# Performance work log

Hardware: AMD Instinct MI355X
Metric: run time of the kernel (lower is better)

The kernel has to match this reference:

```python
import jax, jax.numpy as jnp
import numpy as np


def _scan_dir(x, Wk, Wr, b):
    # x: (B,H,W,C) already flipped for the direction; Wk:(C,4U) Wr:(U,4U) b:(4U,)
    B, H, W, C = x.shape
    U = Wr.shape[0]
    Dmax = min(H, W)          # max anti-diagonal length
    D = H + W - 1             # number of anti-diagonals
    dt = x.dtype
    k = jnp.arange(Dmax)

    def step(carry, d):
        h1, c1, h2, c2 = carry            # diag d-1 and d-2 buffers, (B,Dmax,U)
        i0 = jnp.maximum(0, d - (W - 1))  # first row on diag d
        i1 = jnp.minimum(H - 1, d)        # last row on diag d
        rows = i0 + k
        cols = d - rows
        mask = rows <= i1                 # valid lanes on this diagonal
        rs = jnp.clip(rows, 0, H - 1)
        cs = jnp.clip(cols, 0, W - 1)
        x_diag = x[:, rs, cs, :]          # (B,Dmax,C)
        i0p = jnp.maximum(0, d - W)       # i0 of diag d-1
        i0pp = jnp.maximum(0, d - 1 - W)  # i0 of diag d-2

        def nb(buf, r_nb, lane0, extra):
            v = mask & extra
            lane = jnp.clip(r_nb - lane0, 0, Dmax - 1)
            g = jnp.take(buf, lane, axis=1)
            return jnp.where(v[None, :, None], g, jnp.zeros_like(g)), v

        up_ok = rows - 1 >= 0
        left_ok = cols - 1 >= 0
        h_up, v_up = nb(h1, rows - 1, i0p, up_ok)        # (i-1, j)   on diag d-1
        h_left, v_left = nb(h1, rows, i0p, left_ok)      # (i, j-1)   on diag d-1
        h_ul, v_ul = nb(h2, rows - 1, i0pp, up_ok & left_ok)  # (i-1,j-1) diag d-2
        c_up, _ = nb(c1, rows - 1, i0p, up_ok)
        c_left, _ = nb(c1, rows, i0p, left_ok)
        c_ul, _ = nb(c2, rows - 1, i0pp, up_ok & left_ok)

        cnt = (v_up.astype(dt) + v_left.astype(dt) + v_ul.astype(dt))[None, :, None]
        cnt = jnp.maximum(cnt, jnp.asarray(1.0, dt))
        h_prev = (h_up + h_left + h_ul) / cnt
        c_prev = (c_up + c_left + c_ul) / cnt

        # keras LSTMCell math, gate order i,f,g,o
        z = x_diag @ Wk + h_prev @ Wr + b
        zi, zf, zg, zo = jnp.split(z, 4, axis=-1)
        c_new = jax.nn.sigmoid(zf) * c_prev + jax.nn.sigmoid(zi) * jnp.tanh(zg)
        h_new = jax.nn.sigmoid(zo) * jnp.tanh(c_new)
        m = mask[None, :, None]
        h_new = jnp.where(m, h_new, jnp.zeros_like(h_new))
        c_new = jnp.where(m, c_new, jnp.zeros_like(c_new))
        return (h_new, c_new, h1, c1), h_new

    z0 = jnp.zeros((B, Dmax, U), dt)
    _, hs = jax.lax.scan(step, (z0, z0, z0, z0), jnp.arange(D))  # (D,B,Dmax,U)

    # scatter diagonal buffers back into the (B,H,W,U) grid (static indices)
    d_arr = np.arange(D)[:, None]
    kk = np.arange(Dmax)[None, :]
    rows_all = np.maximum(0, d_arr - (W - 1)) + kk
    cols_all = d_arr - rows_all
    valid = rows_all <= np.minimum(H - 1, d_arr)
    rws = np.where(valid, rows_all, H)   # invalid lanes -> padding row H
    cws = np.where(valid, cols_all, 0)
    out = jnp.zeros((B, H + 1, W, U), dt)
    out = out.at[:, rws, cws].set(jnp.transpose(hs, (1, 0, 2, 3)))
    return out[:, :H]


_FLIPS = [(False, False), (False, True), (True, False), (True, True)]  # SE,SW,NE,NW


def _forward(x, Wk, Wr, b):
    outs = []
    for i, (fh, fw) in enumerate(_FLIPS):
        xx = x
        if fh:
            xx = xx[:, ::-1]
        if fw:
            xx = xx[:, :, ::-1]
        o = _scan_dir(xx, Wk[i], Wr[i], b[i])
        if fw:
            o = o[:, :, ::-1]
        if fh:
            o = o[:, ::-1]
        outs.append(o)
    return jnp.concatenate(outs, axis=-1)


def setup_inputs() -> dict:
    key = jax.random.key(0)
    k0, k1, k2, k3 = jax.random.split(key, 4)
    B, H, W, C, U = 4, 128, 128, 64, 64
    x = jax.random.normal(k0, (B, H, W, C), jnp.float32)
    Wk = jax.random.normal(k1, (4, C, 4 * U), jnp.float32) * 0.08
    Wr = jax.random.normal(k2, (4, U, 4 * U), jnp.float32) * 0.08
    b = jax.random.normal(k3, (4, 4 * U), jnp.float32) * 0.02
    return {"x": x, "Wk": Wk, "Wr": Wr, "b": b}


def reference(x, Wk, Wr, b):
    return _forward(x, Wk, Wr, b)
```

## Files before the change

### kernel.cpp

```cpp
#include <hip/hip_runtime.h>

typedef __bf16 bf16x8 __attribute__((ext_vector_type(8)));
typedef __bf16 bf16x4 __attribute__((ext_vector_type(4)));
typedef float f32x4 __attribute__((ext_vector_type(4)));
typedef unsigned long long u64;

#define NCH 8
#define CELLS 16
#define NG 256
#define L2E 1.44269504089f
#define RDEPTH 16
#define NLINK (16 * 7)
#define RING_U64 (NLINK * RDEPTH * 64)
#define PROG_OFF (RING_U64 * 8)

__device__ __forceinline__ unsigned short f2bfbits(float f) {
  __bf16 b = (__bf16)f;
  return __builtin_bit_cast(unsigned short, b);
}
__device__ __forceinline__ float bfbits2f(unsigned short s) {
  return (float)__builtin_bit_cast(__bf16, s);
}
__device__ __forceinline__ void barrier_lds() {
  asm volatile("s_waitcnt lgkmcnt(0)" ::: "memory");
  __builtin_amdgcn_s_barrier();
}
__device__ __forceinline__ int hix(int row, int byteoff) {
  return row * 128 + (byteoff ^ ((row & 7) << 4));
}

__global__ __launch_bounds__(512, 1) void mdrnn_kernel(
    const float* __restrict__ x, const float* __restrict__ Wk,
    const float* __restrict__ Wr, const float* __restrict__ bias,
    float* __restrict__ out, char* __restrict__ ws) {
  __shared__ __align__(16) unsigned char xt[3][CELLS * 128];
  __shared__ __align__(16) unsigned char Pbuf[2][CELLS * 128];
  __shared__ __align__(16) unsigned char gbh[8 * 128];
  __shared__ __align__(16) float gbc[8 * 64];

  u64* __restrict__ ring = (u64*)ws;
  int* __restrict__ prog = (int*)(ws + PROG_OFF);

  const int tid = threadIdx.x;
  const bool isComp = (tid < 256);
  const int L = tid & 63;
  const int lo16 = L & 15;
  const int hi16 = L >> 4;
  const int wq = (tid >> 6) & 3;
  const int u = wq * 16 + lo16;
  const int hm0 = (tid >> 4) & 15;
  const int hq16 = tid & 15;

  const int ch = blockIdx.x >> 4;
  const int g = blockIdx.x & 15;
  const int f = g >> 2;
  const int bb = g & 3;
  const int fh = (f >> 1) & 1;
  const int fw = f & 1;
  const int R0 = ch * CELLS;
  const int D1 = R0 + 142;
  const int linkDn = g * 7 + ch - 1;
  const int linkUp = g * 7 + ch;

  for (int i = tid; i < 3 * CELLS * 32; i += 512) ((int*)xt)[i] = 0;
  for (int i = tid; i < 2 * CELLS * 32; i += 512) ((int*)Pbuf)[i] = 0;
  for (int i = tid; i < 8 * 32; i += 512) ((int*)gbh)[i] = 0;
  for (int i = tid; i < 8 * 64; i += 512) gbc[i] = 0.f;

  float bsc[4] = {0.f, 0.f, 0.f, 0.f};
  bf16x8 wkh[4][2], wrh[4][2], wrl[4][2];
  int oidx[4];
  int oStep = 0, cbase = 0;
  int o_ph0 = 0, o_ph1 = 0;
  int o_pw[4] = {0, 0, 0, 0};
  if (isComp) {
    const float* Wrf = Wr + f * (64 * NG);
    const float* Wkf = Wk + f * (64 * NG);
#pragma unroll
    for (int t = 0; t < 4; ++t) {
      const float st = (t == 2) ? (2.f * L2E) : L2E;
      bsc[t] = bias[f * NG + t * 64 + u] * st;
#pragma unroll
      for (int kt = 0; kt < 2; ++kt)
#pragma unroll
        for (int jj = 0; jj < 8; ++jj) {
          int k = kt * 32 + hi16 * 8 + jj;
          float vr = Wrf[k * NG + t * 64 + u] * st;
          __bf16 vh = (__bf16)vr;
          wrh[t][kt][jj] = vh;
          wrl[t][kt][jj] = (__bf16)(vr - (float)vh);
          wkh[t][kt][jj] = (__bf16)(Wkf[k * NG + t * 64 + u] * st);
        }
    }
    const int ccStep = fw ? -1 : 1;
#pragma unroll
    for (int j = 0; j < 4; ++j) {
      int ro = R0 + hi16 * 4 + j;
      int rr = fh ? 127 - ro : ro;
      int c0 = R0 - ro;
      oidx[j] = ((bb * 128 + rr) * 128 + (fw ? 127 - c0 : c0)) * NG + f * 64 + u;
      o_pw[j] = hix(hi16 * 4 + j, u * 2);
    }
    oStep = ccStep * NG;
    cbase = -hi16 * 4;
    o_ph0 = hix(lo16, hi16 * 16);
    o_ph1 = hix(lo16, 64 + hi16 * 16);
  }
  const int o_ax0 = hix(lo16, hi16 * 16);
  const int o_ax1 = hix(lo16, 64 + hi16 * 16);

  const int ccStepH = fw ? -1 : 1;
  const int rx = R0 + hm0;
  const int rrx = fh ? 127 - rx : rx;
  int cx = R0 - rx;
  int xidx = ((bb * 128 + rrx) * 128 + (fw ? 127 - cx : cx)) * 64 + hq16 * 4;
  const int xStep = ccStepH * 64;
  float4 px;
  bool pxv = false;
  auto ldg = [&]() {
    pxv = ((unsigned)cx <= 127u);
    px = make_float4(0.f, 0.f, 0.f, 0.f);
    if (pxv) px = *(const float4*)(x + xidx);
    xidx += xStep;
    ++cx;
  };
  auto stx = [&](unsigned char* buf) {
    if (pxv) {
      bf16x4 pk;
      pk[0] = (__bf16)px.x; pk[1] = (__bf16)px.y;
      pk[2] = (__bf16)px.z; pk[3] = (__bf16)px.w;
      *(bf16x4*)(buf + hix(hm0, hq16 * 8)) = pk;
    }
  };

  __syncthreads();

  if (!isComp) {
    ldg();
    stx(&xt[R0 % 3][0]);
    ldg();
  }
  __syncthreads();

  if (!isComp) {
    stx(&xt[(R0 + 1) % 3][0]);
    ldg();
    if (wq == 0 && ch > 0) {
#pragma unroll
      for (int k = 0; k < 2; ++k) {
        const int q = R0 - 1 + k;
        u64* src = ring + ((linkDn * RDEPTH + (q & (RDEPTH - 1))) << 6) + L;
        u64 v;
        int spin = 0;
        for (;;) {
          v = __hip_atomic_load(src, __ATOMIC_RELAXED, __HIP_MEMORY_SCOPE_AGENT);
          if ((unsigned short)(v >> 48) == (unsigned short)q ||
              spin >= (1 << 22))
            break;
          ++spin;
          __builtin_amdgcn_s_sleep(1);
        }
        *(unsigned short*)(gbh + (q & 7) * 128 + L * 2) =
            (unsigned short)(v >> 32);
        gbc[(q & 7) * 64 + L] = __uint_as_float((unsigned)v);
        if (k == 0)
          *(unsigned short*)(&Pbuf[(R0 + 1) & 1][0] + L * 2) =
              (unsigned short)(v >> 32);
      }
      if (L == 0)
        __hip_atomic_store(&prog[linkDn * 16], R0, __ATOMIC_RELAXED,
                           __HIP_MEMORY_SCOPE_AGENT);
    }
  }
  __syncthreads();

  f32x4 zacc[4];
  float hnprev[4];
  float csj[4];
  float puv[4];
  int gateSeen = 0;
  if (isComp) {
    const unsigned char* xp = &xt[R0 % 3][0];
    bf16x8 a0 = *(const bf16x8*)(xp + o_ax0);
    bf16x8 a1 = *(const bf16x8*)(xp + o_ax1);
#pragma unroll
    for (int t = 0; t < 4; ++t) {
      zacc[t] = (f32x4){bsc[t], bsc[t], bsc[t], bsc[t]};
      zacc[t] = __builtin_amdgcn_mfma_f32_16x16x32_bf16(a0, wkh[t][0], zacc[t], 0, 0, 0);
      zacc[t] = __builtin_amdgcn_mfma_f32_16x16x32_bf16(a1, wkh[t][1], zacc[t], 0, 0, 0);
    }
    const float cu0 = gbc[((R0 - 1) & 7) * 64 + u];
#pragma unroll
    for (int j = 0; j < 4; ++j) {
      const float ci = (hi16 == 0 && j == 0) ? cu0 : 0.f;
      csj[j] = ci;
      puv[j] = ci;
      hnprev[j] = 0.f;
    }
    __builtin_amdgcn_s_setprio(1);
  } else {
    stx(&xt[(R0 + 2) % 3][0]);
    ldg();
  }
  __syncthreads();

  unsigned char* Pc = &Pbuf[R0 & 1][0];
  unsigned char* Pp = &Pbuf[(R0 + 1) & 1][0];
  unsigned char* xA = &xt[(R0 + 2) % 3][0];
  unsigned char* xB = &xt[R0 % 3][0];
  unsigned char* xC = &xt[(R0 + 1) % 3][0];

  for (int d = R0; d <= D1; ++d) {
    if (isComp) {
      bf16x8 pa0 = *(const bf16x8*)(Pp + o_ph0);
      bf16x8 pa1 = *(const bf16x8*)(Pp + o_ph1);
      bf16x8 a0 = *(const bf16x8*)(xC + o_ax0);
      bf16x8 a1 = *(const bf16x8*)(xC + o_ax1);
      const float gh1 = bfbits2f(*(const unsigned short*)(gbh + (d & 7) * 128 + u * 2));
      const float gh2 = bfbits2f(*(const unsigned short*)(gbh + ((d - 1) & 7) * 128 + u * 2));
      const float gc1 = gbc[(d & 7) * 64 + u];
#pragma unroll
      for (int t = 0; t < 4; ++t)
        zacc[t] = __builtin_amdgcn_mfma_f32_16x16x32_bf16(pa0, wrh[t][0], zacc[t], 0, 0, 0);
#pragma unroll
      for (int t = 0; t < 4; ++t)
        zacc[t] = __builtin_amdgcn_mfma_f32_16x16x32_bf16(pa1, wrh[t][1], zacc[t], 0, 0, 0);
#pragma unroll
      for (int t = 0; t < 4; ++t)
        zacc[t] = __builtin_amdgcn_mfma_f32_16x16x32_bf16(pa0, wrl[t][0], zacc[t], 0, 0, 0);
#pragma unroll
      for (int t = 0; t < 4; ++t)
        zacc[t] = __builtin_amdgcn_mfma_f32_16x16x32_bf16(pa1, wrl[t][1], zacc[t], 0, 0, 0);

      const bool pubW = (ch < NCH - 1) && (d >= R0 + 15);

      float hcur[4], cnew[4];
      {
        const int cj = cbase - 3;
        const bool ok = ((unsigned)cj <= 127u);
        const float inv = (cj == 0) ? 1.f : (1.f / 3.f);
        const float cpj = csj[3] * inv;
        const float e1 = __builtin_amdgcn_exp2f(-zacc[1][3]);
        const float e2 = __builtin_amdgcn_exp2f(-zacc[0][3]);
        const float e3 = __builtin_amdgcn_exp2f(zacc[2][3]);
        const float A = 1.f + e1, Bv = 1.f + e2, Cv = 1.f + e3;
        const float BC = Bv * Cv;
        float cn = (cpj * BC + (e3 - 1.f) * A) *
                   __builtin_amdgcn_rcpf(A * BC);
        const float e4 = __builtin_amdgcn_exp2f(-zacc[3][3]);
        const float e5 = __builtin_amdgcn_exp2f(2.f * L2E * cn);
        float hn = (e5 - 1.f) * __builtin_amdgcn_rcpf((1.f + e4) * (1.f + e5));
        if (pubW && hi16 == 3) {
          u64 v = ((u64)(unsigned short)d << 48) | ((u64)f2bfbits(hn) << 32) |
                  (u64)__float_as_uint(cn);
          u64* dst = ring + ((linkUp * RDEPTH + (d & (RDEPTH - 1))) << 6) + u;
          __hip_atomic_store(dst, v, __ATOMIC_RELAXED,
                             __HIP_MEMORY_SCOPE_AGENT);
        }
        hcur[3] = ok ? hn : 0.f;
        cnew[3] = ok ? cn : 0.f;
      }
      const unsigned pk =
          ((unsigned)f2bfbits(hcur[3]) << 16) | f2bfbits(hnprev[3]);
      const unsigned pku = __shfl((int)pk, (L - 16) & 63);
      const float up_c = __shfl(cnew[3], (L - 16) & 63);
#pragma unroll
      for (int jj = 0; jj < 3; ++jj) {
        const int j = 2 - jj;
        const int cj = cbase - j;
        const bool ok = ((unsigned)cj <= 127u);
        const float inv =
            (cj == 0 || (j == 0 && R0 == 0 && hi16 == 0)) ? 1.f : (1.f / 3.f);
        const float cpj = csj[j] * inv;
        const float e1 = __builtin_amdgcn_exp2f(-zacc[1][j]);
        const float e2 = __builtin_amdgcn_exp2f(-zacc[0][j]);
        const float e3 = __builtin_amdgcn_exp2f(zacc[2][j]);
        const float A = 1.f + e1, Bv = 1.f + e2, Cv = 1.f + e3;
        const float BC = Bv * Cv;
        float cn = (cpj * BC + (e3 - 1.f) * A) *
                   __builtin_amdgcn_rcpf(A * BC);
        const float e4 = __builtin_amdgcn_exp2f(-zacc[3][j]);
        const float e5 = __builtin_amdgcn_exp2f(2.f * L2E * cn);
        float hn = (e5 - 1.f) * __builtin_amdgcn_rcpf((1.f + e4) * (1.f + e5));
        hcur[j] = ok ? hn : 0.f;
        cnew[j] = ok ? cn : 0.f;
      }
      const float up_h = bfbits2f((unsigned short)(pku >> 16));
      const float up_hp = bfbits2f((unsigned short)(pku & 0xffff));

#pragma unroll
      for (int j = 0; j < 4; ++j) {
        const float hup = j ? hcur[j - 1] : (hi16 ? up_h : gh1);
        const float hulp = j ? hnprev[j - 1] : (hi16 ? up_hp : gh2);
        const float sPj =
            ((cbase + 1 == j) || (R0 == 0 && hi16 == 0 && j == 0))
                ? 1.f : (1.f / 3.f);
        *(unsigned short*)(Pc + o_pw[j]) =
            f2bfbits(sPj * (hup + hcur[j] + hulp));
        const float cun = j ? cnew[j - 1] : (hi16 ? up_c : gc1);
        csj[j] = cun + cnew[j] + puv[j];
        puv[j] = cun;
      }
#pragma unroll
      for (int j = 0; j < 4; ++j) {
        if ((unsigned)(cbase - j) <= 127u) out[oidx[j]] = hcur[j];
        hnprev[j] = hcur[j];
        oidx[j] += oStep;
      }
      ++cbase;

#pragma unroll
      for (int t = 0; t < 4; ++t) {
        zacc[t] = (f32x4){bsc[t], bsc[t], bsc[t], bsc[t]};
        zacc[t] = __builtin_amdgcn_mfma_f32_16x16x32_bf16(a0, wkh[t][0], zacc[t], 0, 0, 0);
        zacc[t] = __builtin_amdgcn_mfma_f32_16x16x32_bf16(a1, wkh[t][1], zacc[t], 0, 0, 0);
      }
    } else {
      const bool meAct = (ch > 0) && (wq == ((d - R0) & 1));
      const int q = d + 1;
      const bool qLive = meAct && (q >= R0 + 1) && (q <= R0 + 126);
      const u64* qs = ring + ((linkDn * RDEPTH + (q & (RDEPTH - 1))) << 6) + L;
      u64 qv = 0;
      if (qLive)
        qv = __hip_atomic_load(qs, __ATOMIC_RELAXED, __HIP_MEMORY_SCOPE_AGENT);
      const int nt = d + 1;
      const bool gatev = (wq == 2) && (ch < NCH - 1) && (nt <= D1) &&
                         (nt >= R0 + 15 + RDEPTH);
      int progNow = gateSeen;
      if (gatev && gateSeen < nt - RDEPTH)
        progNow = __hip_atomic_load(&prog[linkUp * 16], __ATOMIC_RELAXED,
                                    __HIP_MEMORY_SCOPE_AGENT);

      stx(xB);
      ldg();

      if (qLive) {
        int spin = 0;
        while ((unsigned short)(qv >> 48) != (unsigned short)q &&
               spin < (1 << 22)) {
          ++spin;
          __builtin_amdgcn_s_sleep(1);
          qv = __hip_atomic_load(qs, __ATOMIC_RELAXED,
                                 __HIP_MEMORY_SCOPE_AGENT);
        }
        *(unsigned short*)(gbh + (q & 7) * 128 + L * 2) =
            (unsigned short)(qv >> 32);
        gbc[(q & 7) * 64 + L] = __uint_as_float((unsigned)qv);
      }
      if (meAct && L == 0)
        __hip_atomic_store(&prog[linkDn * 16], min(d + 1, R0 + 126),
                           __ATOMIC_RELAXED, __HIP_MEMORY_SCOPE_AGENT);
      if (gatev) {
        if (progNow > gateSeen) gateSeen = progNow;
        int spin = 0;
        while (gateSeen < nt - RDEPTH && spin < (1 << 22)) {
          ++spin;
          __builtin_amdgcn_s_sleep(1);
          gateSeen = __hip_atomic_load(&prog[linkUp * 16], __ATOMIC_RELAXED,
                                       __HIP_MEMORY_SCOPE_AGENT);
        }
      }
    }

    {
      unsigned char* t0 = xA; xA = xB; xB = xC; xC = t0;
      unsigned char* t1 = Pc; Pc = Pp; Pp = t1;
    }
    barrier_lds();
  }
}

extern "C" void kernel_launch(void* const* d_in, const int* in_sizes, int n_in,
                              void* d_out, int out_size, void* d_ws, size_t ws_size,
                              hipStream_t stream) {
  const float* x = (const float*)d_in[0];
  const float* Wk = (const float*)d_in[1];
  const float* Wr = (const float*)d_in[2];
  const float* b = (const float*)d_in[3];
  float* out = (float*)d_out;
  hipMemsetAsync(d_ws, 0, PROG_OFF + NLINK * 16 * sizeof(int), stream);
  hipLaunchKernelGGL(mdrnn_kernel, dim3(128), dim3(512), 0, stream, x, Wk, Wr,
                     b, out, (char*)d_ws);
}
```

Baseline: 222.9 us.

## Drop helper warps; compute warps load x from global and poll ring directly

Removes the 256 producer threads that staged x into LDS and polled the inter-block ring, leaving a 256-thread block. Each compute lane now issues its own global float4 loads of x for the next diagonal, packs them to bf16 in registers for the MFMA input, and polls the ring for boundary h/c values held in registers. This removes the xt/gbh/gbc LDS buffers and their staging, aiming to cut LDS traffic and barrier work per step. In exchange, global load latency and spin-waits now sit on the critical compute path and x is loaded redundantly across lanes.

```diff
diff --git a/kernel.cpp b/kernel.cpp
--- a/kernel.cpp
+++ b/kernel.cpp
@@ -1,7 +1,6 @@
 #include <hip/hip_runtime.h>
 
 typedef __bf16 bf16x8 __attribute__((ext_vector_type(8)));
-typedef __bf16 bf16x4 __attribute__((ext_vector_type(4)));
 typedef float f32x4 __attribute__((ext_vector_type(4)));
 typedef unsigned long long u64;
 
@@ -28,28 +27,34 @@
 __device__ __forceinline__ int hix(int row, int byteoff) {
   return row * 128 + (byteoff ^ ((row & 7) << 4));
 }
-
-__global__ __launch_bounds__(512, 1) void mdrnn_kernel(
+__device__ __forceinline__ bf16x8 pack8(float4 a, float4 b, bool v) {
+  bf16x8 r;
+  r[0] = (__bf16)(v ? a.x : 0.f);
+  r[1] = (__bf16)(v ? a.y : 0.f);
+  r[2] = (__bf16)(v ? a.z : 0.f);
+  r[3] = (__bf16)(v ? a.w : 0.f);
+  r[4] = (__bf16)(v ? b.x : 0.f);
+  r[5] = (__bf16)(v ? b.y : 0.f);
+  r[6] = (__bf16)(v ? b.z : 0.f);
+  r[7] = (__bf16)(v ? b.w : 0.f);
+  return r;
+}
+
+__global__ __launch_bounds__(256, 1) void mdrnn_kernel(
     const float* __restrict__ x, const float* __restrict__ Wk,
     const float* __restrict__ Wr, const float* __restrict__ bias,
     float* __restrict__ out, char* __restrict__ ws) {
-  __shared__ __align__(16) unsigned char xt[3][CELLS * 128];
   __shared__ __align__(16) unsigned char Pbuf[2][CELLS * 128];
-  __shared__ __align__(16) unsigned char gbh[8 * 128];
-  __shared__ __align__(16) float gbc[8 * 64];
 
   u64* __restrict__ ring = (u64*)ws;
   int* __restrict__ prog = (int*)(ws + PROG_OFF);
 
   const int tid = threadIdx.x;
-  const bool isComp = (tid < 256);
   const int L = tid & 63;
   const int lo16 = L & 15;
   const int hi16 = L >> 4;
-  const int wq = (tid >> 6) & 3;
+  const int wq = tid >> 6;
   const int u = wq * 16 + lo16;
-  const int hm0 = (tid >> 4) & 15;
-  const int hq16 = tid & 15;
 
   const int ch = blockIdx.x >> 4;
   const int g = blockIdx.x & 15;
@@ -62,18 +67,11 @@
   const int linkDn = g * 7 + ch - 1;
   const int linkUp = g * 7 + ch;
 
-  for (int i = tid; i < 3 * CELLS * 32; i += 512) ((int*)xt)[i] = 0;
-  for (int i = tid; i < 2 * CELLS * 32; i += 512) ((int*)Pbuf)[i] = 0;
-  for (int i = tid; i < 8 * 32; i += 512) ((int*)gbh)[i] = 0;
-  for (int i = tid; i < 8 * 64; i += 512) gbc[i] = 0.f;
-
-  float bsc[4] = {0.f, 0.f, 0.f, 0.f};
+  for (int i = tid; i < 2 * CELLS * 32; i += 256) ((int*)Pbuf)[i] = 0;
+
+  float bsc[4];
   bf16x8 wkh[4][2], wrh[4][2], wrl[4][2];
-  int oidx[4];
-  int oStep = 0, cbase = 0;
-  int o_ph0 = 0, o_ph1 = 0;
-  int o_pw[4] = {0, 0, 0, 0};
-  if (isComp) {
+  {
     const float* Wrf = Wr + f * (64 * NG);
     const float* Wkf = Wk + f * (64 * NG);
 #pragma unroll
@@ -92,278 +90,247 @@
           wkh[t][kt][jj] = (__bf16)(Wkf[k * NG + t * 64 + u] * st);
         }
     }
-    const int ccStep = fw ? -1 : 1;
-#pragma unroll
-    for (int j = 0; j < 4; ++j) {
-      int ro = R0 + hi16 * 4 + j;
-      int rr = fh ? 127 - ro : ro;
-      int c0 = R0 - ro;
-      oidx[j] = ((bb * 128 + rr) * 128 + (fw ? 127 - c0 : c0)) * NG + f * 64 + u;
-      o_pw[j] = hix(hi16 * 4 + j, u * 2);
-    }
-    oStep = ccStep * NG;
-    cbase = -hi16 * 4;
-    o_ph0 = hix(lo16, hi16 * 16);
-    o_ph1 = hix(lo16, 64 + hi16 * 16);
-  }
-  const int o_ax0 = hix(lo16, hi16 * 16);
-  const int o_ax1 = hix(lo16, 64 + hi16 * 16);
-
-  const int ccStepH = fw ? -1 : 1;
-  const int rx = R0 + hm0;
-  const int rrx = fh ? 127 - rx : rx;
-  int cx = R0 - rx;
-  int xidx = ((bb * 128 + rrx) * 128 + (fw ? 127 - cx : cx)) * 64 + hq16 * 4;
-  const int xStep = ccStepH * 64;
-  float4 px;
-  bool pxv = false;
-  auto ldg = [&]() {
-    pxv = ((unsigned)cx <= 127u);
-    px = make_float4(0.f, 0.f, 0.f, 0.f);
-    if (pxv) px = *(const float4*)(x + xidx);
-    xidx += xStep;
-    ++cx;
-  };
-  auto stx = [&](unsigned char* buf) {
-    if (pxv) {
-      bf16x4 pk;
-      pk[0] = (__bf16)px.x; pk[1] = (__bf16)px.y;
-      pk[2] = (__bf16)px.z; pk[3] = (__bf16)px.w;
-      *(bf16x4*)(buf + hix(hm0, hq16 * 8)) = pk;
-    }
-  };
+  }
+  int oidx[4], o_pw[4];
+  const int ccStep = fw ? -1 : 1;
+#pragma unroll
+  for (int j = 0; j < 4; ++j) {
+    int ro = R0 + hi16 * 4 + j;
+    int rr = fh ? 127 - ro : ro;
+    int c0 = R0 - ro;
+    oidx[j] = ((bb * 128 + rr) * 128 + (fw ? 127 - c0 : c0)) * NG + f * 64 + u;
+    o_pw[j] = hix(hi16 * 4 + j, u * 2);
+  }
+  const int oStep = ccStep * NG;
+  int cbase = -hi16 * 4;
+  const int o_ph0 = hix(lo16, hi16 * 16);
+  const int o_ph1 = hix(lo16, 64 + hi16 * 16);
+
+  const int xr = R0 + lo16;
+  const int rrx = fh ? 127 - xr : xr;
+  const float* xrow = x + ((bb * 128 + rrx) * 128) * 64 + hi16 * 8;
 
   __syncthreads();
 
-  if (!isComp) {
-    ldg();
-    stx(&xt[R0 % 3][0]);
-    ldg();
-  }
-  __syncthreads();
-
-  if (!isComp) {
-    stx(&xt[(R0 + 1) % 3][0]);
-    ldg();
-    if (wq == 0 && ch > 0) {
-#pragma unroll
-      for (int k = 0; k < 2; ++k) {
-        const int q = R0 - 1 + k;
-        u64* src = ring + ((linkDn * RDEPTH + (q & (RDEPTH - 1))) << 6) + L;
-        u64 v;
-        int spin = 0;
-        for (;;) {
-          v = __hip_atomic_load(src, __ATOMIC_RELAXED, __HIP_MEMORY_SCOPE_AGENT);
-          if ((unsigned short)(v >> 48) == (unsigned short)q ||
-              spin >= (1 << 22))
-            break;
-          ++spin;
-          __builtin_amdgcn_s_sleep(1);
-        }
-        *(unsigned short*)(gbh + (q & 7) * 128 + L * 2) =
+  float g_h = 0.f, g_c = 0.f, gh2 = 0.f, cu0 = 0.f;
+  int gateSeen = 0;
+  if (ch > 0 && hi16 == 0) {
+#pragma unroll
+    for (int k = 0; k < 2; ++k) {
+      const int q = R0 - 1 + k;
+      const u64* src = ring + ((linkDn * RDEPTH + (q & (RDEPTH - 1))) << 6) + u;
+      u64 v;
+      int spin = 0;
+      for (;;) {
+        v = __hip_atomic_load(src, __ATOMIC_RELAXED, __HIP_MEMORY_SCOPE_AGENT);
+        if ((unsigned short)(v >> 48) == (unsigned short)q ||
+            spin >= (1 << 22))
+          break;
+        ++spin;
+        __builtin_amdgcn_s_sleep(1);
+      }
+      if (k == 0) {
+        gh2 = bfbits2f((unsigned short)(v >> 32));
+        cu0 = __uint_as_float((unsigned)v);
+        *(unsigned short*)(&Pbuf[(R0 + 1) & 1][0] + u * 2) =
             (unsigned short)(v >> 32);
-        gbc[(q & 7) * 64 + L] = __uint_as_float((unsigned)v);
-        if (k == 0)
-          *(unsigned short*)(&Pbuf[(R0 + 1) & 1][0] + L * 2) =
-              (unsigned short)(v >> 32);
-      }
-      if (L == 0)
-        __hip_atomic_store(&prog[linkDn * 16], R0, __ATOMIC_RELAXED,
-                           __HIP_MEMORY_SCOPE_AGENT);
-    }
-  }
-  __syncthreads();
+      } else {
+        g_h = bfbits2f((unsigned short)(v >> 32));
+        g_c = __uint_as_float((unsigned)v);
+      }
+    }
+    if (tid == 0)
+      __hip_atomic_store(&prog[linkDn * 16], R0, __ATOMIC_RELAXED,
+                         __HIP_MEMORY_SCOPE_AGENT);
+  }
 
   f32x4 zacc[4];
-  float hnprev[4];
-  float csj[4];
-  float puv[4];
-  int gateSeen = 0;
-  if (isComp) {
-    const unsigned char* xp = &xt[R0 % 3][0];
-    bf16x8 a0 = *(const bf16x8*)(xp + o_ax0);
-    bf16x8 a1 = *(const bf16x8*)(xp + o_ax1);
+  {
+    const bool xv = (lo16 == 0);
+    const int cc = fw ? 127 : 0;
+    const float* xp = xrow + cc * 64;
+    float4 A0 = *(const float4*)(xp);
+    float4 A1 = *(const float4*)(xp + 4);
+    float4 B0 = *(const float4*)(xp + 32);
+    float4 B1 = *(const float4*)(xp + 36);
+    bf16x8 a0 = pack8(A0, A1, xv);
+    bf16x8 a1 = pack8(B0, B1, xv);
 #pragma unroll
     for (int t = 0; t < 4; ++t) {
       zacc[t] = (f32x4){bsc[t], bsc[t], bsc[t], bsc[t]};
       zacc[t] = __builtin_amdgcn_mfma_f32_16x16x32_bf16(a0, wkh[t][0], zacc[t], 0, 0, 0);
       zacc[t] = __builtin_amdgcn_mfma_f32_16x16x32_bf16(a1, wkh[t][1], zacc[t], 0, 0, 0);
     }
-    const float cu0 = gbc[((R0 - 1) & 7) * 64 + u];
-#pragma unroll
-    for (int j = 0; j < 4; ++j) {
-      const float ci = (hi16 == 0 && j == 0) ? cu0 : 0.f;
-      csj[j] = ci;
-      puv[j] = ci;
-      hnprev[j] = 0.f;
-    }
-    __builtin_amdgcn_s_setprio(1);
-  } else {
-    stx(&xt[(R0 + 2) % 3][0]);
-    ldg();
+  }
+  float hnprev[4], csj[4], puv[4];
+#pragma unroll
+  for (int j = 0; j < 4; ++j) {
+    const float ci = (hi16 == 0 && j == 0) ? cu0 : 0.f;
+    csj[j] = ci;
+    puv[j] = ci;
+    hnprev[j] = 0.f;
   }
   __syncthreads();
 
   unsigned char* Pc = &Pbuf[R0 & 1][0];
   unsigned char* Pp = &Pbuf[(R0 + 1) & 1][0];
-  unsigned char* xA = &xt[(R0 + 2) % 3][0];
-  unsigned char* xB = &xt[R0 % 3][0];
-  unsigned char* xC = &xt[(R0 + 1) % 3][0];
 
   for (int d = R0; d <= D1; ++d) {
-    if (isComp) {
-      bf16x8 pa0 = *(const bf16x8*)(Pp + o_ph0);
-      bf16x8 pa1 = *(const bf16x8*)(Pp + o_ph1);
-      bf16x8 a0 = *(const bf16x8*)(xC + o_ax0);
-      bf16x8 a1 = *(const bf16x8*)(xC + o_ax1);
-      const float gh1 = bfbits2f(*(const unsigned short*)(gbh + (d & 7) * 128 + u * 2));
-      const float gh2 = bfbits2f(*(const unsigned short*)(gbh + ((d - 1) & 7) * 128 + u * 2));
-      const float gc1 = gbc[(d & 7) * 64 + u];
-#pragma unroll
-      for (int t = 0; t < 4; ++t)
-        zacc[t] = __builtin_amdgcn_mfma_f32_16x16x32_bf16(pa0, wrh[t][0], zacc[t], 0, 0, 0);
-#pragma unroll
-      for (int t = 0; t < 4; ++t)
-        zacc[t] = __builtin_amdgcn_mfma_f32_16x16x32_bf16(pa1, wrh[t][1], zacc[t], 0, 0, 0);
-#pragma unroll
-      for (int t = 0; t < 4; ++t)
-        zacc[t] = __builtin_amdgcn_mfma_f32_16x16x32_bf16(pa0, wrl[t][0], zacc[t], 0, 0, 0);
-#pragma unroll
-      for (int t = 0; t < 4; ++t)
-        zacc[t] = __builtin_amdgcn_mfma_f32_16x16x32_bf16(pa1, wrl[t][1], zacc[t], 0, 0, 0);
-
-      const bool pubW = (ch < NCH - 1) && (d >= R0 + 15);
-
-      float hcur[4], cnew[4];
-      {
-        const int cj = cbase - 3;
-        const bool ok = ((unsigned)cj <= 127u);
-        const float inv = (cj == 0) ? 1.f : (1.f / 3.f);
-        const float cpj = csj[3] * inv;
-        const float e1 = __builtin_amdgcn_exp2f(-zacc[1][3]);
-        const float e2 = __builtin_amdgcn_exp2f(-zacc[0][3]);
-        const float e3 = __builtin_amdgcn_exp2f(zacc[2][3]);
-        const float A = 1.f + e1, Bv = 1.f + e2, Cv = 1.f + e3;
-        const float BC = Bv * Cv;
-        float cn = (cpj * BC + (e3 - 1.f) * A) *
-                   __builtin_amdgcn_rcpf(A * BC);
-        const float e4 = __builtin_amdgcn_exp2f(-zacc[3][3]);
-        const float e5 = __builtin_amdgcn_exp2f(2.f * L2E * cn);
-        float hn = (e5 - 1.f) * __builtin_amdgcn_rcpf((1.f + e4) * (1.f + e5));
-        if (pubW && hi16 == 3) {
-          u64 v = ((u64)(unsigned short)d << 48) | ((u64)f2bfbits(hn) << 32) |
-                  (u64)__float_as_uint(cn);
-          u64* dst = ring + ((linkUp * RDEPTH + (d & (RDEPTH - 1))) << 6) + u;
-          __hip_atomic_store(dst, v, __ATOMIC_RELAXED,
-                             __HIP_MEMORY_SCOPE_AGENT);
-        }
-        hcur[3] = ok ? hn : 0.f;
-        cnew[3] = ok ? cn : 0.f;
-      }
-      const unsigned pk =
-          ((unsigned)f2bfbits(hcur[3]) << 16) | f2bfbits(hnprev[3]);
-      const unsigned pku = __shfl((int)pk, (L - 16) & 63);
-      const float up_c = __shfl(cnew[3], (L - 16) & 63);
-#pragma unroll
-      for (int jj = 0; jj < 3; ++jj) {
-        const int j = 2 - jj;
-        const int cj = cbase - j;
-        const bool ok = ((unsigned)cj <= 127u);
-        const float inv =
-            (cj == 0 || (j == 0 && R0 == 0 && hi16 == 0)) ? 1.f : (1.f / 3.f);
-        const float cpj = csj[j] * inv;
-        const float e1 = __builtin_amdgcn_exp2f(-zacc[1][j]);
-        const float e2 = __builtin_amdgcn_exp2f(-zacc[0][j]);
-        const float e3 = __builtin_amdgcn_exp2f(zacc[2][j]);
-        const float A = 1.f + e1, Bv = 1.f + e2, Cv = 1.f + e3;
-        const float BC = Bv * Cv;
-        float cn = (cpj * BC + (e3 - 1.f) * A) *
-                   __builtin_amdgcn_rcpf(A * BC);
-        const float e4 = __builtin_amdgcn_exp2f(-zacc[3][j]);
-        const float e5 = __builtin_amdgcn_exp2f(2.f * L2E * cn);
-        float hn = (e5 - 1.f) * __builtin_amdgcn_rcpf((1.f + e4) * (1.f + e5));
-        hcur[j] = ok ? hn : 0.f;
-        cnew[j] = ok ? cn : 0.f;
-      }
-      const float up_h = bfbits2f((unsigned short)(pku >> 16));
-      const float up_hp = bfbits2f((unsigned short)(pku & 0xffff));
-
-#pragma unroll
-      for (int j = 0; j < 4; ++j) {
-        const float hup = j ? hcur[j - 1] : (hi16 ? up_h : gh1);
-        const float hulp = j ? hnprev[j - 1] : (hi16 ? up_hp : gh2);
-        const float sPj =
-            ((cbase + 1 == j) || (R0 == 0 && hi16 == 0 && j == 0))
-                ? 1.f : (1.f / 3.f);
-        *(unsigned short*)(Pc + o_pw[j]) =
-            f2bfbits(sPj * (hup + hcur[j] + hulp));
-        const float cun = j ? cnew[j - 1] : (hi16 ? up_c : gc1);
-        csj[j] = cun + cnew[j] + puv[j];
-        puv[j] = cun;
-      }
-#pragma unroll
-      for (int j = 0; j < 4; ++j) {
-        if ((unsigned)(cbase - j) <= 127u) out[oidx[j]] = hcur[j];
-        hnprev[j] = hcur[j];
-        oidx[j] += oStep;
-      }
-      ++cbase;
-
+    const int cN = (d + 1) - xr;
+    const bool xv = ((unsigned)cN <= 127u);
+    const int ccl = cN < 0 ? 0 : (cN > 127 ? 127 : cN);
+    const int cc = fw ? 127 - ccl : ccl;
+    const float* xp = xrow + cc * 64;
+    const float4 XA0 = *(const float4*)(xp);
+    const float4 XA1 = *(const float4*)(xp + 4);
+    const float4 XB0 = *(const float4*)(xp + 32);
+    const float4 XB1 = *(const float4*)(xp + 36);
+
+    const int q = d + 1;
+    const bool qLive = (ch > 0) && (hi16 == 0) && (q <= R0 + 126);
+    const u64* qs = ring + ((linkDn * RDEPTH + (q & (RDEPTH - 1))) << 6) + u;
+    u64 qv = 0;
+    if (qLive)
+      qv = __hip_atomic_load(qs, __ATOMIC_RELAXED, __HIP_MEMORY_SCOPE_AGENT);
+
+    const int nt = d + 1;
+    const bool gatev = (tid == 0) && (ch < NCH - 1) && (nt <= D1) &&
+                       (nt >= R0 + 15 + RDEPTH);
+    int progNow = gateSeen;
+    if (gatev && gateSeen < nt - RDEPTH)
+      progNow = __hip_atomic_load(&prog[linkUp * 16], __ATOMIC_RELAXED,
+                                  __HIP_MEMORY_SCOPE_AGENT);
+
+    bf16x8 pa0 = *(const bf16x8*)(Pp + o_ph0);
+    bf16x8 pa1 = *(const bf16x8*)(Pp + o_ph1);
+    const float gh1 = g_h;
+    const float gc1 = g_c;
+#pragma unroll
+    for (int t = 0; t < 4; ++t)
+      zacc[t] = __builtin_amdgcn_mfma_f32_16x16x32_bf16(pa0, wrh[t][0], zacc[t], 0, 0, 0);
+#pragma unroll
+    for (int t = 0; t < 4; ++t)
+      zacc[t] = __builtin_amdgcn_mfma_f32_16x16x32_bf16(pa1, wrh[t][1], zacc[t], 0, 0, 0);
+#pragma unroll
+    for (int t = 0; t < 4; ++t)
+      zacc[t] = __builtin_amdgcn_mfma_f32_16x16x32_bf16(pa0, wrl[t][0], zacc[t], 0, 0, 0);
+#pragma unroll
+    for (int t = 0; t < 4; ++t)
+      zacc[t] = __builtin_amdgcn_mfma_f32_16x16x32_bf16(pa1, wrl[t][1], zacc[t], 0, 0, 0);
+
+    const bool pubW = (ch < NCH - 1) && (d >= R0 + 15);
+
+    float hcur[4], cnew[4];
+    {
+      const int cj = cbase - 3;
+      const bool ok = ((unsigned)cj <= 127u);
+      const float inv = (cj == 0) ? 1.f : (1.f / 3.f);
+      const float cpj = csj[3] * inv;
+      const float e1 = __builtin_amdgcn_exp2f(-zacc[1][3]);
+      const float e2 = __builtin_amdgcn_exp2f(-zacc[0][3]);
+      const float e3 = __builtin_amdgcn_exp2f(zacc[2][3]);
+      const float A = 1.f + e1, Bv = 1.f + e2, Cv = 1.f + e3;
+      const float BC = Bv * Cv;
+      float cn = (cpj * BC + (e3 - 1.f) * A) * __builtin_amdgcn_rcpf(A * BC);
+      const float e4 = __builtin_amdgcn_exp2f(-zacc[3][3]);
+      const float e5 = __builtin_amdgcn_exp2f(2.f * L2E * cn);
+      float hn = (e5 - 1.f) * __builtin_amdgcn_rcpf((1.f + e4) * (1.f + e5));
+      if (pubW && hi16 == 3) {
+        u64 v = ((u64)(unsigned short)d << 48) | ((u64)f2bfbits(hn) << 32) |
+                (u64)__float_as_uint(cn);
+        u64* dst = ring + ((linkUp * RDEPTH + (d & (RDEPTH - 1))) << 6) + u;
+        __hip_atomic_store(dst, v, __ATOMIC_RELAXED, __HIP_MEMORY_SCOPE_AGENT);
+      }
+      hcur[3] = ok ? hn : 0.f;
+      cnew[3] = ok ? cn : 0.f;
+    }
+    const unsigned pk =
+        ((unsigned)f2bfbits(hcur[3]) << 16) | f2bfbits(hnprev[3]);
+    const unsigned pku = __shfl((int)pk, (L - 16) & 63);
+    const float up_c = __shfl(cnew[3], (L - 16) & 63);
+#pragma unroll
+    for (int jj = 0; jj < 3; ++jj) {
+      const int j = 2 - jj;
+      const int cj = cbase - j;
+      const bool ok = ((unsigned)cj <= 127u);
+      const float inv =
+          (cj == 0 || (j == 0 && R0 == 0 && hi16 == 0)) ? 1.f : (1.f / 3.f);
+      const float cpj = csj[j] * inv;
+      const float e1 = __builtin_amdgcn_exp2f(-zacc[1][j]);
+      const float e2 = __builtin_amdgcn_exp2f(-zacc[0][j]);
+      const float e3 = __builtin_amdgcn_exp2f(zacc[2][j]);
+      const float A = 1.f + e1, Bv = 1.f + e2, Cv = 1.f + e3;
+      const float BC = Bv * Cv;
+      float cn = (cpj * BC + (e3 - 1.f) * A) * __builtin_amdgcn_rcpf(A * BC);
+      const float e4 = __builtin_amdgcn_exp2f(-zacc[3][j]);
+      const float e5 = __builtin_amdgcn_exp2f(2.f * L2E * cn);
+      float hn = (e5 - 1.f) * __builtin_amdgcn_rcpf((1.f + e4) * (1.f + e5));
+      hcur[j] = ok ? hn : 0.f;
+      cnew[j] = ok ? cn : 0.f;
+    }
+    const float up_h = bfbits2f((unsigned short)(pku >> 16));
+    const float up_hp = bfbits2f((unsigned short)(pku & 0xffff));
+
+#pragma unroll
+    for (int j = 0; j < 4; ++j) {
+      const float hup = j ? hcur[j - 1] : (hi16 ? up_h : gh1);
+      const float hulp = j ? hnprev[j - 1] : (hi16 ? up_hp : gh2);
+      const float sPj =
+          ((cbase + 1 == j) || (R0 == 0 && hi16 == 0 && j == 0))
+              ? 1.f : (1.f / 3.f);
+      *(unsigned short*)(Pc + o_pw[j]) =
+          f2bfbits(sPj * (hup + hcur[j] + hulp));
+      const float cun = j ? cnew[j - 1] : (hi16 ? up_c : gc1);
+      csj[j] = cun + cnew[j] + puv[j];
+      puv[j] = cun;
+    }
+    gh2 = gh1;
+
+#pragma unroll
+    for (int j = 0; j < 4; ++j) {
+      if ((unsigned)(cbase - j) <= 127u) out[oidx[j]] = hcur[j];
+      hnprev[j] = hcur[j];
+      oidx[j] += oStep;
+    }
+    ++cbase;
+
+    {
+      bf16x8 a0 = pack8(XA0, XA1, xv);
+      bf16x8 a1 = pack8(XB0, XB1, xv);
 #pragma unroll
       for (int t = 0; t < 4; ++t) {
         zacc[t] = (f32x4){bsc[t], bsc[t], bsc[t], bsc[t]};
         zacc[t] = __builtin_amdgcn_mfma_f32_16x16x32_bf16(a0, wkh[t][0], zacc[t], 0, 0, 0);
         zacc[t] = __builtin_amdgcn_mfma_f32_16x16x32_bf16(a1, wkh[t][1], zacc[t], 0, 0, 0);
       }
-    } else {
-      const bool meAct = (ch > 0) && (wq == ((d - R0) & 1));
-      const int q = d + 1;
-      const bool qLive = meAct && (q >= R0 + 1) && (q <= R0 + 126);
-      const u64* qs = ring + ((linkDn * RDEPTH + (q & (RDEPTH - 1))) << 6) + L;
-      u64 qv = 0;
-      if (qLive)
+    }
+
+    if (qLive) {
+      int spin = 0;
+      while ((unsigned short)(qv >> 48) != (unsigned short)q &&
+             spin < (1 << 22)) {
+        ++spin;
+        __builtin_amdgcn_s_sleep(1);
         qv = __hip_atomic_load(qs, __ATOMIC_RELAXED, __HIP_MEMORY_SCOPE_AGENT);
-      const int nt = d + 1;
-      const bool gatev = (wq == 2) && (ch < NCH - 1) && (nt <= D1) &&
-                         (nt >= R0 + 15 + RDEPTH);
-      int progNow = gateSeen;
-      if (gatev && gateSeen < nt - RDEPTH)
-        progNow = __hip_atomic_load(&prog[linkUp * 16], __ATOMIC_RELAXED,
-                                    __HIP_MEMORY_SCOPE_AGENT);
-
-      stx(xB);
-      ldg();
-
-      if (qLive) {
-        int spin = 0;
-        while ((unsigned short)(qv >> 48) != (unsigned short)q &&
-               spin < (1 << 22)) {
-          ++spin;
-          __builtin_amdgcn_s_sleep(1);
-          qv = __hip_atomic_load(qs, __ATOMIC_RELAXED,
-                                 __HIP_MEMORY_SCOPE_AGENT);
-        }
-        *(unsigned short*)(gbh + (q & 7) * 128 + L * 2) =
-            (unsigned short)(qv >> 32);
-        gbc[(q & 7) * 64 + L] = __uint_as_float((unsigned)qv);
-      }
-      if (meAct && L == 0)
-        __hip_atomic_store(&prog[linkDn * 16], min(d + 1, R0 + 126),
-                           __ATOMIC_RELAXED, __HIP_MEMORY_SCOPE_AGENT);
-      if (gatev) {
-        if (progNow > gateSeen) gateSeen = progNow;
-        int spin = 0;
-        while (gateSeen < nt - RDEPTH && spin < (1 << 22)) {
-          ++spin;
-          __builtin_amdgcn_s_sleep(1);
-          gateSeen = __hip_atomic_load(&prog[linkUp * 16], __ATOMIC_RELAXED,
-                                       __HIP_MEMORY_SCOPE_AGENT);
-        }
+      }
+      g_h = bfbits2f((unsigned short)(qv >> 32));
+      g_c = __uint_as_float((unsigned)qv);
+    }
+    if (ch > 0 && tid == 0)
+      __hip_atomic_store(&prog[linkDn * 16], min(d + 1, R0 + 126),
+                         __ATOMIC_RELAXED, __HIP_MEMORY_SCOPE_AGENT);
+    if (gatev) {
+      if (progNow > gateSeen) gateSeen = progNow;
+      int spin = 0;
+      while (gateSeen < nt - RDEPTH && spin < (1 << 22)) {
+        ++spin;
+        __builtin_amdgcn_s_sleep(1);
+        gateSeen = __hip_atomic_load(&prog[linkUp * 16], __ATOMIC_RELAXED,
+                                     __HIP_MEMORY_SCOPE_AGENT);
       }
     }
 
     {
-      unsigned char* t0 = xA; xA = xB; xB = xC; xC = t0;
       unsigned char* t1 = Pc; Pc = Pp; Pp = t1;
     }
     barrier_lds();
@@ -379,6 +346,6 @@
   const float* b = (const float*)d_in[3];
   float* out = (float*)d_out;
   hipMemsetAsync(d_ws, 0, PROG_OFF + NLINK * 16 * sizeof(int), stream);
-  hipLaunchKernelGGL(mdrnn_kernel, dim3(128), dim3(512), 0, stream, x, Wk, Wr,
+  hipLaunchKernelGGL(mdrnn_kernel, dim3(128), dim3(256), 0, stream, x, Wk, Wr,
                      b, out, (char*)d_ws);
 }
```

Measured after the change: 331.5 us. 1.49x slower.
